# Performance work log

Hardware: AMD Instinct MI355X
Metric: run time of the kernel (lower is better)

Reference implementation:

```python
import jax, jax.numpy as jnp
import numpy as np

NUM_EXPERTS = 8
TOP_K = 2
HIDDEN = 1024
INTER_TOTAL = 8192  # intermediate_size * experts_per_rank
B, S = 2, 2048


def setup_inputs() -> dict:
    key = jax.random.key(0)
    k1, k2, k3, k4, k5, k6 = jax.random.split(key, 6)
    T = B * S
    x = jax.random.normal(k1, (B, S, HIDDEN), dtype=jnp.float32)
    scores = jax.random.uniform(k2, (T, NUM_EXPERTS), dtype=jnp.float32)
    expert_weights = jax.random.uniform(k3, (T, TOP_K), dtype=jnp.float32)
    top_experts = jax.random.randint(k4, (T, TOP_K), 0, NUM_EXPERTS, dtype=jnp.int32)
    w1 = jax.random.normal(k5, (HIDDEN, INTER_TOTAL), dtype=jnp.float32) * 0.02
    w2 = jax.random.normal(k6, (INTER_TOTAL, HIDDEN), dtype=jnp.float32) * 0.02
    return {"x": x, "scores": scores, "expert_weights": expert_weights,
            "top_experts": top_experts, "w1": w1, "w2": w2}


def reference(x, scores, expert_weights, top_experts, w1, w2):
    # forward_once with expert_parallel_size == 1 (dropless MoE dispatch/combine).
    in_shape = x.shape
    T = in_shape[0] * in_shape[1]
    H = in_shape[-1]
    x_flat = x.reshape(T, H)

    flat_experts = top_experts.reshape(-1)          # [T*top_k]
    flat_weights = expert_weights.reshape(-1)       # [T*top_k]

    # ops.sort: stable radix sort of routed copies by expert id
    order = jnp.argsort(flat_experts, stable=True)  # "indices"
    token_idx = order // TOP_K                      # source token per sorted slot

    # padded_gather: bucket tokens per expert (padding rows are zeros and
    # pass through the bias-free MLP as zeros, so they never affect output)
    xg = x_flat[token_idx]                          # [T*top_k, H]

    # MLP: w1 -> gelu(tanh approx) -> w2
    h = jax.nn.gelu(xg @ w1, approximate=True)      # [T*top_k, inter*E]
    y = h @ w2                                      # [T*top_k, H]

    # padded_scatter: weighted combine back to token order
    w_sorted = flat_weights[order]
    out = jnp.zeros((T, H), dtype=x.dtype).at[token_idx].add(w_sorted[:, None] * y)
    return out.reshape(in_shape)
```

## Files before the change

### kernel.cpp

```cpp
#include <hip/hip_runtime.h>
#include <hip/hip_bf16.h>
#include <math.h>

#define HID 1024
#define INTER 8192
#define TT 4096

typedef __bf16 bf16x8 __attribute__((ext_vector_type(8)));
typedef float f32x4 __attribute__((ext_vector_type(4)));

__device__ __forceinline__ void gll16(const void* g, void* l) {
    __builtin_amdgcn_global_load_lds(
        (const __attribute__((address_space(1))) void*)g,
        (__attribute__((address_space(3))) void*)l, 16, 0, 0);
}

template <int OFF>
__device__ __forceinline__ bf16x8 ds_read128o(unsigned addr) {
    bf16x8 r;
    asm volatile("ds_read_b128 %0, %1 offset:%c2" : "=v"(r) : "v"(addr), "i"(OFF));
    return r;
}

__device__ __forceinline__ void tcast_tile(const float* __restrict__ in,
                                           __hip_bfloat16* __restrict__ out,
                                           int R, int C, int bx, int by, int tid) {
    __shared__ float tile[32][33];
    const int tx = tid & 31, ty = tid >> 5;
    const int br = by * 32, bc = bx * 32;
#pragma unroll
    for (int j = 0; j < 32; j += 8)
        tile[ty + j][tx] = in[(size_t)(br + ty + j) * C + bc + tx];
    __syncthreads();
#pragma unroll
    for (int j = 0; j < 32; j += 8)
        out[(size_t)(bc + ty + j) * R + br + tx] = __float2bfloat16(tile[tx][ty + j]);
}

__global__ void k_prep(const float* __restrict__ x, const float* __restrict__ ew,
                       const float* __restrict__ w1, const float* __restrict__ w2,
                       __hip_bfloat16* __restrict__ xb, float* __restrict__ s,
                       __hip_bfloat16* __restrict__ w1t, __hip_bfloat16* __restrict__ w2t) {
    const int bid = blockIdx.x, tid = threadIdx.x;
    if (bid < 1024) {
        const int n4 = (TT * HID) / 4;
        const int stride = 1024 * 256;
        for (int i = bid * 256 + tid; i < n4; i += stride) {
            float4 v = ((const float4*)x)[i];
            __hip_bfloat16* o = xb + (size_t)i * 4;
            o[0] = __float2bfloat16(v.x);
            o[1] = __float2bfloat16(v.y);
            o[2] = __float2bfloat16(v.z);
            o[3] = __float2bfloat16(v.w);
        }
        for (int t = bid * 256 + tid; t < TT; t += stride)
            s[t] = ew[2 * t] + ew[2 * t + 1];
    } else if (bid < 1024 + 8192) {
        const int b = bid - 1024;
        tcast_tile(w1, w1t, HID, INTER, b % 256, b / 256, tid);
    } else {
        const int b = bid - (1024 + 8192);
        tcast_tile(w2, w2t, INTER, HID, b % 32, b / 32, tid);
    }
}

template <int EPI>
__global__ __launch_bounds__(512, 2) void k_gemm1b(
    const __hip_bfloat16* __restrict__ A, const __hip_bfloat16* __restrict__ Bt,
    __hip_bfloat16* __restrict__ hOut, float* __restrict__ fOut,
    const float* __restrict__ s, int Kfull, int nt, int Nout) {
    __shared__ __hip_bfloat16 sA[2][2][128][64];
    __shared__ __hip_bfloat16 sB[2][2][128][64];
    const int tid = threadIdx.x;
    const int lane = tid & 63, wid = tid >> 6;
    const int wr = wid >> 2, wc = wid & 3;

    const int nwg = gridDim.x * gridDim.y;
    const int wg = blockIdx.y * gridDim.x + blockIdx.x;
    const int swz = (wg & 7) * (nwg >> 3) + (wg >> 3);
    const int brow = (swz / gridDim.x) * 256;
    const int bcol = (swz % gridDim.x) * 256;
    const size_t kbase = (size_t)blockIdx.z * ((size_t)nt * 64);

    const int colsw = (((lane & 7) ^ (lane >> 3)) << 3);
    const int qA0 = (wid & 3) * 4;
    const int bh = (wid >> 1) & 1;
    const int qB0 = ((wid & 1) | ((wid >> 2) << 1)) * 4;
    const __hip_bfloat16* gA2 =
        A + (size_t)(brow + wr * 128 + qA0 * 8 + (lane >> 3)) * Kfull + kbase + colsw;
    const __hip_bfloat16* gB2 =
        Bt + (size_t)(bcol + bh * 128 + qB0 * 8 + (lane >> 3)) * Kfull + kbase + colsw;
    char* ldsA2 = (char*)&sA[0][0][0][0] + wr * 16384 + qA0 * 1024;
    char* ldsB2 = (char*)&sB[0][0][0][0] + bh * 16384 + qB0 * 1024;
    const size_t chunkStep = (size_t)8 * Kfull;

    const unsigned baseA = (unsigned)(uintptr_t)&sA[0][0][0][0];
    const unsigned baseB = (unsigned)(uintptr_t)&sB[0][0][0][0];
    const unsigned g0 = (((lane >> 4)) ^ (lane & 7)) << 4;
    const unsigned g1 = ((4 + (lane >> 4)) ^ (lane & 7)) << 4;
    const unsigned rdA0 = baseA + wr * 16384 + (lane & 15) * 128 + g0;
    const unsigned rdA1 = baseA + wr * 16384 + (lane & 15) * 128 + g1;
    const unsigned rdB0 = baseB + (wc >> 1) * 16384 + (wc & 1) * 8192 + (lane & 15) * 128 + g0;
    const unsigned rdB1 = baseB + (wc >> 1) * 16384 + (wc & 1) * 8192 + (lane & 15) * 128 + g1;

    f32x4 acc[8][4] = {};
    bf16x8 a03[4][2], a47[4][2], b01[2][2], b23[2][2];

#define STAGE_A2(bufoff, t)                                                    \
    do {                                                                       \
        _Pragma("unroll") for (int j = 0; j < 4; ++j)                          \
            gll16(gA2 + (size_t)j * chunkStep + (size_t)(t) * 64,              \
                  ldsA2 + (bufoff) + j * 1024);                                \
    } while (0)
#define STAGE_B2(bufoff, t)                                                    \
    do {                                                                       \
        _Pragma("unroll") for (int j = 0; j < 4; ++j)                          \
            gll16(gB2 + (size_t)j * chunkStep + (size_t)(t) * 64,              \
                  ldsB2 + (bufoff) + j * 1024);                                \
    } while (0)
#define PIN() __builtin_amdgcn_sched_barrier(0)
#define BAR()                              \
    do {                                   \
        PIN();                             \
        __builtin_amdgcn_s_barrier();      \
        PIN();                             \
    } while (0)
#define WAIT_LG12() __builtin_amdgcn_s_waitcnt(0xCC7F)
#define WAIT_LG8() __builtin_amdgcn_s_waitcnt(0xC87F)
#define WAIT_LG0() __builtin_amdgcn_s_waitcnt(0xC07F)
#define WAIT_VM0() __builtin_amdgcn_s_waitcnt(0x0F70)

    STAGE_A2(0u, 0);
    STAGE_B2(0u, 0);
    WAIT_VM0();
    BAR();

#pragma unroll 1
    for (int i = 0; i < nt; ++i) {
        const unsigned co = (i & 1) ? 32768u : 0u;
        const unsigned no = co ^ 32768u;
        const bool full = (i + 1 < nt);
        const unsigned aA0 = rdA0 + co, aA1 = rdA1 + co;
        const unsigned aB0 = rdB0 + co, aB1 = rdB1 + co;

        a03[0][0] = ds_read128o<0>(aA0);
        a03[0][1] = ds_read128o<0>(aA1);
        a03[1][0] = ds_read128o<2048>(aA0);
        a03[1][1] = ds_read128o<2048>(aA1);
        a03[2][0] = ds_read128o<4096>(aA0);
        a03[2][1] = ds_read128o<4096>(aA1);
        a03[3][0] = ds_read128o<6144>(aA0);
        a03[3][1] = ds_read128o<6144>(aA1);
        b01[0][0] = ds_read128o<0>(aB0);
        b01[0][1] = ds_read128o<0>(aB1);
        b01[1][0] = ds_read128o<2048>(aB0);
        b01[1][1] = ds_read128o<2048>(aB1);
        b23[0][0] = ds_read128o<4096>(aB0);
        b23[0][1] = ds_read128o<4096>(aB1);
        b23[1][0] = ds_read128o<6144>(aB0);
        b23[1][1] = ds_read128o<6144>(aB1);
        a47[0][0] = ds_read128o<8192>(aA0);
        a47[0][1] = ds_read128o<8192>(aA1);
        a47[1][0] = ds_read128o<10240>(aA0);
        a47[1][1] = ds_read128o<10240>(aA1);
        a47[2][0] = ds_read128o<12288>(aA0);
        a47[2][1] = ds_read128o<12288>(aA1);
        a47[3][0] = ds_read128o<14336>(aA0);
        a47[3][1] = ds_read128o<14336>(aA1);

        if (full) {
            STAGE_A2(no, i + 1);
            STAGE_B2(no, i + 1);
        }

        __builtin_amdgcn_s_setprio(1);
        WAIT_LG12();
        PIN();
#pragma unroll
        for (int ks = 0; ks < 2; ++ks)
#pragma unroll
            for (int m = 0; m < 4; ++m)
#pragma unroll
                for (int n = 0; n < 2; ++n)
                    acc[m][n] = __builtin_amdgcn_mfma_f32_16x16x32_bf16(
                        a03[m][ks], b01[n][ks], acc[m][n], 0, 0, 0);
        PIN();
        WAIT_LG8();
        PIN();
#pragma unroll
        for (int ks = 0; ks < 2; ++ks)
#pragma unroll
            for (int m = 0; m < 4; ++m)
#pragma unroll
                for (int n = 0; n < 2; ++n)
                    acc[m][2 + n] = __builtin_amdgcn_mfma_f32_16x16x32_bf16(
                        a03[m][ks], b23[n][ks], acc[m][2 + n], 0, 0, 0);
        PIN();
        WAIT_LG0();
        PIN();
#pragma unroll
        for (int ks = 0; ks < 2; ++ks)
#pragma unroll
            for (int m = 0; m < 4; ++m)
#pragma unroll
                for (int n = 0; n < 2; ++n)
                    acc[4 + m][2 + n] = __builtin_amdgcn_mfma_f32_16x16x32_bf16(
                        a47[m][ks], b23[n][ks], acc[4 + m][2 + n], 0, 0, 0);
#pragma unroll
        for (int ks = 0; ks < 2; ++ks)
#pragma unroll
            for (int m = 0; m < 4; ++m)
#pragma unroll
                for (int n = 0; n < 2; ++n)
                    acc[4 + m][n] = __builtin_amdgcn_mfma_f32_16x16x32_bf16(
                        a47[m][ks], b01[n][ks], acc[4 + m][n], 0, 0, 0);
        __builtin_amdgcn_s_setprio(0);
        PIN();
        WAIT_VM0();
        BAR();
    }

    const int orow = brow + wr * 128 + ((lane >> 4) << 2);
    const int ocol = bcol + wc * 64 + (lane & 15);
#pragma unroll
    for (int m = 0; m < 8; ++m) {
#pragma unroll
        for (int j = 0; j < 4; ++j) {
            const int r = orow + m * 16 + j;
            const size_t ro = (size_t)r * Nout;
            if (EPI == 0) {
#pragma unroll
                for (int n = 0; n < 4; ++n) {
                    float v = acc[m][n][j];
                    float u = 1.5957691216057308f * (v + 0.044715f * v * v * v);
                    float g = v / (1.0f + __expf(-u));
                    hOut[ro + ocol + n * 16] = __float2bfloat16(g);
                }
            } else {
                const float sc = s[r];
#pragma unroll
                for (int n = 0; n < 4; ++n)
                    unsafeAtomicAdd(&fOut[ro + ocol + n * 16], sc * acc[m][n][j]);
            }
        }
    }
#undef STAGE_A2
#undef STAGE_B2
#undef PIN
#undef BAR
#undef WAIT_LG12
#undef WAIT_LG8
#undef WAIT_LG0
#undef WAIT_VM0
}

extern "C" void kernel_launch(void* const* d_in, const int* in_sizes, int n_in,
                              void* d_out, int out_size, void* d_ws, size_t ws_size,
                              hipStream_t stream) {
    const float* x = (const float*)d_in[0];
    const float* ew = (const float*)d_in[2];
    const float* w1 = (const float*)d_in[4];
    const float* w2 = (const float*)d_in[5];
    float* out = (float*)d_out;

    char* ws = (char*)d_ws;
    float* s = (float*)ws;
    __hip_bfloat16* xb = (__hip_bfloat16*)(ws + 16384);
    __hip_bfloat16* w1t = (__hip_bfloat16*)(ws + 16384 + 8388608);
    __hip_bfloat16* w2t = (__hip_bfloat16*)(ws + 16384 + 8388608 + 16777216);
    __hip_bfloat16* h = (__hip_bfloat16*)(ws + 16384 + 8388608 + 2 * 16777216);

    k_prep<<<1024 + 8192 + 8192, 256, 0, stream>>>(x, ew, w1, w2, xb, s, w1t, w2t);

    dim3 g1(INTER / 256, TT / 256, 1);
    k_gemm1b<0><<<g1, 512, 0, stream>>>(xb, w1t, h, nullptr, nullptr, HID, HID / 64, INTER);

    hipMemsetAsync(out, 0, (size_t)TT * HID * sizeof(float), stream);
    dim3 g2(HID / 256, TT / 256, 4);
    k_gemm1b<1><<<g2, 512, 0, stream>>>(h, w2t, nullptr, out, s, INTER, 2048 / 64, HID);
}
```

Measured before the change: 198.9 us.

## Fuse w2 transpose and output zeroing into GEMM1 with smaller 128x128 tiles

Moves the w2 fp32-to-bf16 transpose and the output zeroing out of the prep kernel and the memset, and into extra blocks appended to the first GEMM launch, so they run alongside the GEMM tiles. GEMM1 is rewritten as a dedicated kernel with 128x128 tiles, 256 threads, and a 2-stage LDS buffer, giving 2048 tiles instead of 512. This removes a memset launch, shortens prep, and may improve load balance. The trade-off is a smaller tile with less data reuse per block, and the extra blocks compete with the GEMM for CUs.

```diff
diff --git a/kernel.cpp b/kernel.cpp
--- a/kernel.cpp
+++ b/kernel.cpp
@@ -22,10 +22,10 @@
     return r;
 }
 
-__device__ __forceinline__ void tcast_tile(const float* __restrict__ in,
-                                           __hip_bfloat16* __restrict__ out,
-                                           int R, int C, int bx, int by, int tid) {
-    __shared__ float tile[32][33];
+__device__ __forceinline__ void tcast_tile_p(const float* __restrict__ in,
+                                             __hip_bfloat16* __restrict__ out,
+                                             int R, int C, int bx, int by, int tid,
+                                             float (*tile)[33]) {
     const int tx = tid & 31, ty = tid >> 5;
     const int br = by * 32, bc = bx * 32;
 #pragma unroll
@@ -35,12 +35,14 @@
 #pragma unroll
     for (int j = 0; j < 32; j += 8)
         out[(size_t)(bc + ty + j) * R + br + tx] = __float2bfloat16(tile[tx][ty + j]);
+    __syncthreads();
 }
 
 __global__ void k_prep(const float* __restrict__ x, const float* __restrict__ ew,
-                       const float* __restrict__ w1, const float* __restrict__ w2,
+                       const float* __restrict__ w1,
                        __hip_bfloat16* __restrict__ xb, float* __restrict__ s,
-                       __hip_bfloat16* __restrict__ w1t, __hip_bfloat16* __restrict__ w2t) {
+                       __hip_bfloat16* __restrict__ w1t) {
+    __shared__ float tile[32][33];
     const int bid = blockIdx.x, tid = threadIdx.x;
     if (bid < 1024) {
         const int n4 = (TT * HID) / 4;
@@ -55,20 +57,171 @@
         }
         for (int t = bid * 256 + tid; t < TT; t += stride)
             s[t] = ew[2 * t] + ew[2 * t + 1];
-    } else if (bid < 1024 + 8192) {
+    } else {
         const int b = bid - 1024;
-        tcast_tile(w1, w1t, HID, INTER, b % 256, b / 256, tid);
-    } else {
-        const int b = bid - (1024 + 8192);
-        tcast_tile(w2, w2t, INTER, HID, b % 32, b / 32, tid);
-    }
-}
-
-template <int EPI>
-__global__ __launch_bounds__(512, 2) void k_gemm1b(
+        tcast_tile_p(w1, w1t, HID, INTER, b % 256, b / 256, tid, tile);
+    }
+}
+
+__global__ __launch_bounds__(256, 2) void k_g1f(
     const __hip_bfloat16* __restrict__ A, const __hip_bfloat16* __restrict__ Bt,
-    __hip_bfloat16* __restrict__ hOut, float* __restrict__ fOut,
-    const float* __restrict__ s, int Kfull, int nt, int Nout) {
+    __hip_bfloat16* __restrict__ hOut,
+    const float* __restrict__ w2, __hip_bfloat16* __restrict__ w2t,
+    float* __restrict__ outZ, int Kfull, int nt, int Nout) {
+    __shared__ __hip_bfloat16 sA[2][128][64];
+    __shared__ __hip_bfloat16 sB[2][128][64];
+    __shared__ float tile[32][33];
+    const int tid = threadIdx.x;
+
+    if (blockIdx.x >= 2048) {
+        const int ab = blockIdx.x - 2048;
+        float4* o4 = (float4*)outZ;
+        const int N4 = (TT * HID) / 4;
+        for (int i = ab * 256 + tid; i < N4; i += 2048 * 256)
+            o4[i] = make_float4(0.f, 0.f, 0.f, 0.f);
+#pragma unroll 1
+        for (int t = ab * 4; t < ab * 4 + 4; ++t)
+            tcast_tile_p(w2, w2t, INTER, HID, t % 32, t / 32, tid, tile);
+        return;
+    }
+
+    const int lane = tid & 63, wid = tid >> 6;
+    const int wr = wid >> 1, wc = wid & 1;
+
+    const int wg = blockIdx.x;
+    const int swz = (wg & 7) * 256 + (wg >> 3);
+    const int brow = (swz / 64) * 128;
+    const int bcol = (swz % 64) * 128;
+
+    const int colsw = (((lane & 7) ^ (lane >> 3)) << 3);
+    const __hip_bfloat16* gA2 =
+        A + (size_t)(brow + wid * 32 + (lane >> 3)) * Kfull + colsw;
+    const __hip_bfloat16* gB2 =
+        Bt + (size_t)(bcol + wid * 32 + (lane >> 3)) * Kfull + colsw;
+    char* ldsA2 = (char*)&sA[0][0][0] + wid * 4096;
+    char* ldsB2 = (char*)&sB[0][0][0] + wid * 4096;
+    const size_t chunkStep = (size_t)8 * Kfull;
+
+    const unsigned baseA = (unsigned)(uintptr_t)&sA[0][0][0];
+    const unsigned baseB = (unsigned)(uintptr_t)&sB[0][0][0];
+    const unsigned g0 = (((lane >> 4)) ^ (lane & 7)) << 4;
+    const unsigned g1 = ((4 + (lane >> 4)) ^ (lane & 7)) << 4;
+    const unsigned rdA0 = baseA + wr * 8192 + (lane & 15) * 128 + g0;
+    const unsigned rdA1 = baseA + wr * 8192 + (lane & 15) * 128 + g1;
+    const unsigned rdB0 = baseB + wc * 8192 + (lane & 15) * 128 + g0;
+    const unsigned rdB1 = baseB + wc * 8192 + (lane & 15) * 128 + g1;
+
+    f32x4 acc[4][4] = {};
+    bf16x8 aF[4], b01[2], b23[2];
+
+#define STAGE_AB(bufoff, t)                                                    \
+    do {                                                                       \
+        _Pragma("unroll") for (int j = 0; j < 4; ++j)                          \
+            gll16(gA2 + (size_t)j * chunkStep + (size_t)(t) * 64,              \
+                  ldsA2 + (bufoff) + j * 1024);                                \
+        _Pragma("unroll") for (int j = 0; j < 4; ++j)                          \
+            gll16(gB2 + (size_t)j * chunkStep + (size_t)(t) * 64,              \
+                  ldsB2 + (bufoff) + j * 1024);                                \
+    } while (0)
+#define PIN() __builtin_amdgcn_sched_barrier(0)
+#define BAR()                              \
+    do {                                   \
+        PIN();                             \
+        __builtin_amdgcn_s_barrier();      \
+        PIN();                             \
+    } while (0)
+#define WAIT_LG4() __builtin_amdgcn_s_waitcnt(0xC47F)
+#define WAIT_LG0() __builtin_amdgcn_s_waitcnt(0xC07F)
+#define WAIT_VM0() __builtin_amdgcn_s_waitcnt(0x0F70)
+
+    STAGE_AB(0u, 0);
+    WAIT_VM0();
+    BAR();
+
+    bf16x8 aQ[4], bQ01[2], bQ23[2];
+    (void)aQ; (void)bQ01; (void)bQ23;
+#pragma unroll 1
+    for (int i = 0; i < nt; ++i) {
+        const unsigned co = (i & 1) ? 16384u : 0u;
+        const unsigned no = co ^ 16384u;
+        const bool full = (i + 1 < nt);
+        const unsigned aA0 = rdA0 + co, aA1 = rdA1 + co;
+        const unsigned aB0 = rdB0 + co, aB1 = rdB1 + co;
+
+        aF[0] = ds_read128o<0>(aA0);
+        aF[1] = ds_read128o<2048>(aA0);
+        aF[2] = ds_read128o<4096>(aA0);
+        aF[3] = ds_read128o<6144>(aA0);
+        b01[0] = ds_read128o<0>(aB0);
+        b01[1] = ds_read128o<2048>(aB0);
+        b23[0] = ds_read128o<4096>(aB0);
+        b23[1] = ds_read128o<6144>(aB0);
+        aQ[0] = ds_read128o<0>(aA1);
+        aQ[1] = ds_read128o<2048>(aA1);
+        aQ[2] = ds_read128o<4096>(aA1);
+        aQ[3] = ds_read128o<6144>(aA1);
+        bQ01[0] = ds_read128o<0>(aB1);
+        bQ01[1] = ds_read128o<2048>(aB1);
+        bQ23[0] = ds_read128o<4096>(aB1);
+        bQ23[1] = ds_read128o<6144>(aB1);
+
+        if (full) STAGE_AB(no, i + 1);
+
+        __builtin_amdgcn_s_setprio(1);
+        WAIT_LG4();
+        PIN();
+#pragma unroll
+        for (int m = 0; m < 4; ++m) {
+            acc[m][0] = __builtin_amdgcn_mfma_f32_16x16x32_bf16(aF[m], b01[0], acc[m][0], 0, 0, 0);
+            acc[m][1] = __builtin_amdgcn_mfma_f32_16x16x32_bf16(aF[m], b01[1], acc[m][1], 0, 0, 0);
+            acc[m][2] = __builtin_amdgcn_mfma_f32_16x16x32_bf16(aF[m], b23[0], acc[m][2], 0, 0, 0);
+            acc[m][3] = __builtin_amdgcn_mfma_f32_16x16x32_bf16(aF[m], b23[1], acc[m][3], 0, 0, 0);
+        }
+        PIN();
+        WAIT_LG0();
+        PIN();
+#pragma unroll
+        for (int m = 0; m < 4; ++m) {
+            acc[m][0] = __builtin_amdgcn_mfma_f32_16x16x32_bf16(aQ[m], bQ01[0], acc[m][0], 0, 0, 0);
+            acc[m][1] = __builtin_amdgcn_mfma_f32_16x16x32_bf16(aQ[m], bQ01[1], acc[m][1], 0, 0, 0);
+            acc[m][2] = __builtin_amdgcn_mfma_f32_16x16x32_bf16(aQ[m], bQ23[0], acc[m][2], 0, 0, 0);
+            acc[m][3] = __builtin_amdgcn_mfma_f32_16x16x32_bf16(aQ[m], bQ23[1], acc[m][3], 0, 0, 0);
+        }
+        __builtin_amdgcn_s_setprio(0);
+        PIN();
+        WAIT_VM0();
+        BAR();
+    }
+
+    const int orow = brow + wr * 64 + ((lane >> 4) << 2);
+    const int ocol = bcol + wc * 64 + (lane & 15);
+#pragma unroll
+    for (int m = 0; m < 4; ++m) {
+#pragma unroll
+        for (int j = 0; j < 4; ++j) {
+            const int r = orow + m * 16 + j;
+            const size_t ro = (size_t)r * Nout;
+#pragma unroll
+            for (int n = 0; n < 4; ++n) {
+                float v = acc[m][n][j];
+                float u = 1.5957691216057308f * (v + 0.044715f * v * v * v);
+                float g = v / (1.0f + __expf(-u));
+                hOut[ro + ocol + n * 16] = __float2bfloat16(g);
+            }
+        }
+    }
+#undef STAGE_AB
+#undef PIN
+#undef BAR
+#undef WAIT_LG4
+#undef WAIT_LG0
+#undef WAIT_VM0
+}
+
+__global__ __launch_bounds__(512, 2) void k_gemm2(
+    const __hip_bfloat16* __restrict__ A, const __hip_bfloat16* __restrict__ Bt,
+    float* __restrict__ fOut, const float* __restrict__ s, int Kfull, int nt,
+    int Nout) {
     __shared__ __hip_bfloat16 sA[2][2][128][64];
     __shared__ __hip_bfloat16 sB[2][2][128][64];
     const int tid = threadIdx.x;
@@ -228,20 +381,10 @@
         for (int j = 0; j < 4; ++j) {
             const int r = orow + m * 16 + j;
             const size_t ro = (size_t)r * Nout;
-            if (EPI == 0) {
-#pragma unroll
-                for (int n = 0; n < 4; ++n) {
-                    float v = acc[m][n][j];
-                    float u = 1.5957691216057308f * (v + 0.044715f * v * v * v);
-                    float g = v / (1.0f + __expf(-u));
-                    hOut[ro + ocol + n * 16] = __float2bfloat16(g);
-                }
-            } else {
-                const float sc = s[r];
-#pragma unroll
-                for (int n = 0; n < 4; ++n)
-                    unsafeAtomicAdd(&fOut[ro + ocol + n * 16], sc * acc[m][n][j]);
-            }
+            const float sc = s[r];
+#pragma unroll
+            for (int n = 0; n < 4; ++n)
+                unsafeAtomicAdd(&fOut[ro + ocol + n * 16], sc * acc[m][n][j]);
         }
     }
 #undef STAGE_A2
@@ -270,12 +413,10 @@
     __hip_bfloat16* w2t = (__hip_bfloat16*)(ws + 16384 + 8388608 + 16777216);
     __hip_bfloat16* h = (__hip_bfloat16*)(ws + 16384 + 8388608 + 2 * 16777216);
 
-    k_prep<<<1024 + 8192 + 8192, 256, 0, stream>>>(x, ew, w1, w2, xb, s, w1t, w2t);
-
-    dim3 g1(INTER / 256, TT / 256, 1);
-    k_gemm1b<0><<<g1, 512, 0, stream>>>(xb, w1t, h, nullptr, nullptr, HID, HID / 64, INTER);
-
-    hipMemsetAsync(out, 0, (size_t)TT * HID * sizeof(float), stream);
+    k_prep<<<1024 + 8192, 256, 0, stream>>>(x, ew, w1, xb, s, w1t);
+
+    k_g1f<<<4096, 256, 0, stream>>>(xb, w1t, h, w2, w2t, out, HID, HID / 64, INTER);
+
     dim3 g2(HID / 256, TT / 256, 4);
-    k_gemm1b<1><<<g2, 512, 0, stream>>>(h, w2t, nullptr, out, s, INTER, 2048 / 64, HID);
-}
+    k_gemm2<<<g2, 512, 0, stream>>>(h, w2t, out, s, INTER, 2048 / 64, HID);
+}
```

Measured after the change: 216.6 us. +8.9%, slower.
